# Kernel tuning notes

Hardware: AMD Instinct MI355X
Metric: run time of the kernel (lower is better)

## Reference

```python
import jax, jax.numpy as jnp
import numpy as np

SMOOTH = 1.0      # self.smooth
NUM_ITER = 10     # iter_
EPS = 1e-07
INF = 1e12        # stand-in for +inf in squared-distance init


def _maxpool(x, window):
    # torch max_pool3d(stride=1, padding=w//2): pad with -inf, window max
    pads = ((0, 0), (0, 0)) + tuple((w // 2, w // 2) for w in window)
    return jax.lax.reduce_window(x, -jnp.inf, jax.lax.max, (1, 1) + window, (1, 1, 1, 1, 1), pads)


def _soft_erode(x):  # x: [B,1,D,H,W]
    p1 = -_maxpool(-x, (3, 1, 1))
    p2 = -_maxpool(-x, (1, 3, 1))
    p3 = -_maxpool(-x, (1, 1, 3))
    return jnp.minimum(jnp.minimum(p1, p2), p3)


def _soft_open(x):
    return _maxpool(_soft_erode(x), (3, 3, 3))  # dilate(erode(x))


def _soft_skel(x, n_iter):
    skel = jax.nn.relu(x - _soft_open(x))
    for _ in range(n_iter):
        x = _soft_erode(x)
        delta = jax.nn.relu(x - _soft_open(x))
        skel = skel + jax.nn.relu(delta - skel * delta)
    return skel


def _edt_pass(d2, axis):
    # 1D squared-distance min-convolution: out[i] = min_j (i-j)^2 + d2[j]
    L = d2.shape[axis]
    d2m = jnp.moveaxis(d2, axis, -1)                 # [..., L]
    i = jnp.arange(L, dtype=d2.dtype)
    sq = (i[:, None] - i[None, :]) ** 2              # [L, L]
    out = jnp.min(d2m[..., None, :] + sq, axis=-1)   # [..., L]
    return jnp.moveaxis(out, -1, axis)


def _edt(mask):
    # exact Euclidean distance transform: distance of nonzero voxels to nearest zero voxel
    d2 = jnp.where(mask > 0, INF, 0.0).astype(jnp.float32)  # [B,D,H,W]
    for ax in (1, 2, 3):
        d2 = _edt_pass(d2, ax)
    return jnp.sqrt(d2)


def _get_weights(mask, skel):
    # mask, skel: [B,D,H,W] binary float
    dist = _edt(mask)
    dist = jnp.where(mask == 0, 0.0, dist)
    on_skel = skel == 1
    skel_r = jnp.where(on_skel, dist, 0.0)
    rmax = jnp.max(skel_r.reshape(skel_r.shape[0], -1), axis=1).reshape(-1, 1, 1, 1)
    valid = rmax > 0
    rmax_safe = jnp.where(valid, rmax, 1.0)
    dist_n = jnp.where(valid, dist / rmax_safe, dist)
    skel_rn = jnp.where(valid, skel_r / rmax_safe, skel_r)
    # dim == 3 branch: skel_1_R2_norm
    skel_1r2 = jnp.where(on_skel, (1.0 + EPS) / (skel_rn ** 2 + EPS), 0.0)
    return dist_n, skel_rn, skel_1r2


def _combine(A, B, C):
    # D = B*C, overwritten by A*C where (A != 0) & (B == 0)
    return jnp.where((A != 0) & (B == 0), A * C, B * C)


def reference(y_pred, y_true):
    # y_pred: [B,C,D,H,W] logits; y_true: [B,1,D,H,W] int labels
    fore = jnp.max(y_pred[:, 1:], axis=1, keepdims=True)
    logits = jnp.concatenate([y_pred[:, :1], fore], axis=1)   # [B,2,D,H,W]
    prob = jax.nn.softmax(logits, axis=1)
    yp = (prob[:, 1] > 0.5).astype(jnp.float32)               # [B,D,H,W]
    yt = (y_true > 0).astype(jnp.float32)[:, 0]               # [B,D,H,W]

    skel_p = _soft_skel(yp[:, None], NUM_ITER)[:, 0]
    skel_t = _soft_skel(yt[:, None], NUM_ITER)[:, 0]

    q_vl, q_slvl, q_sl = _get_weights(yt, skel_t)
    q_vp, q_spvp, q_sp = _get_weights(yp, skel_p)

    w_tprec = (jnp.sum(q_sp * q_vl) + SMOOTH) / (jnp.sum(_combine(q_spvp, q_slvl, q_sp)) + SMOOTH)
    w_tsens = (jnp.sum(q_sl * q_vp) + SMOOTH) / (jnp.sum(_combine(q_slvl, q_spvp, q_sl)) + SMOOTH)
    return 1.0 - 2.0 * (w_tprec * w_tsens) / (w_tprec + w_tsens)


def setup_inputs() -> dict:
    key = jax.random.key(0)
    k1, k2 = jax.random.split(key)
    y_pred = jax.random.normal(k1, (2, 2, 64, 96, 96), dtype=jnp.float32)
    y_true = jax.random.randint(k2, (2, 1, 64, 96, 96), 0, 2, dtype=jnp.int32)
    return {"y_pred": y_pred, "y_true": y_true}
```

## Files before the change

### kernel.cpp

```cpp
#include <hip/hip_runtime.h>

namespace {

constexpr int Bn = 2;
constexpr int Dn = 64;
constexpr int Hn = 96;
constexpr int Wn = 96;
constexpr int HW = Hn * Wn;
constexpr int S  = Dn * HW;
constexpr int NBS = Bn * S;
constexpr int NT  = 2 * NBS;
constexpr int WPP = HW / 32;
constexpr int WPS = S / 32;
constexpr int NTW = NT / 32;
constexpr float EPSf = 1e-7f;
constexpr int BLK_SUMS = NBS / 4 / 256;
#define BIGF 1e12f
constexpr int LINF = 1 << 20;

__global__ __launch_bounds__(256) void k_bin0(const float* __restrict__ logits,
                                              const int* __restrict__ labels,
                                              unsigned short* __restrict__ FZ,
                                              unsigned char* __restrict__ DZ) {
  __shared__ unsigned bits[64];
  __shared__ unsigned zlo[32], zhi[32];
  int slab = blockIdx.x / 288;
  int cg = blockIdx.x - slab * 288;
  int c0 = cg * 32;
  int tid = threadIdx.x;
  int lane = tid & 63;
  for (int t = tid; t < 2048; t += 256) {
    int zz = t >> 5;
    int col = t & 31;
    int s = zz * HW + c0 + col;
    bool v;
    if (slab < 2) {
      float l0 = logits[(slab * 2 + 0) * S + s];
      float l1 = logits[(slab * 2 + 1) * S + s];
      v = l1 > l0;
    } else {
      v = labels[(slab - 2) * S + s] > 0;
    }
    unsigned long long m = __ballot(v);
    if (lane == 0)       bits[zz] = (unsigned)m;
    else if (lane == 32) bits[zz] = (unsigned)(m >> 32);
  }
  __syncthreads();
  if (tid < 64) {
    int col = tid & 31;
    int base = (tid < 32) ? 0 : 32;
    unsigned zw = 0u;
    #pragma unroll
    for (int j = 0; j < 32; ++j)
      zw |= (((bits[base + j] >> col) & 1u) ^ 1u) << j;
    if (tid < 32) zlo[col] = zw; else zhi[col] = zw;
  }
  __syncthreads();
  int col = tid & 31;
  int chunk = tid >> 5;
  int i0 = chunk * 8;
  unsigned long long Z = ((unsigned long long)zhi[col] << 32) | (unsigned long long)zlo[col];
  unsigned short* o = FZ + slab * S + c0 + col;
  unsigned char* o1 = DZ + slab * S + c0 + col;
  #pragma unroll
  for (int s = 0; s < 8; ++s) {
    int i = i0 + s;
    unsigned long long below = Z & ((2ull << i) - 1ull);
    unsigned long long above = Z >> i;
    unsigned short fv;
    unsigned char dv;
    if (below | above) {
      int ddn = below ? (i - (63 - __builtin_clzll(below))) : 99;
      int dup = above ? __builtin_ctzll(above) : 99;
      int d = ddn < dup ? ddn : dup;
      fv = (unsigned short)(d * d);
      dv = (unsigned char)d;
    } else {
      fv = 0xFFFFu;
      dv = 255;
    }
    o[i * HW] = fv;
    o1[i * HW] = dv;
  }
}

__global__ __launch_bounds__(256) void k_edtl1(const unsigned short* __restrict__ FZ,
                                               const unsigned char* __restrict__ DZ,
                                               float* __restrict__ EF,
                                               unsigned char* __restrict__ D1) {
  __shared__ __align__(16) unsigned shm[8640];
  unsigned short* fz = (unsigned short*)shm;
  unsigned char*  dz = (unsigned char*)(shm + 4608);
  unsigned char*  t1 = (unsigned char*)(shm + 6912);
  unsigned short* o1 = (unsigned short*)(shm + 7488);
  unsigned short* Afwd = (unsigned short*)shm;
  unsigned short* Bbwd = (unsigned short*)(shm + 4608);
  int slab = blockIdx.x >> 8;
  int z = (blockIdx.x >> 2) & 63;
  int y0 = (blockIdx.x & 3) * 24;
  int tid = threadIdx.x;
  int pb = slab * S + z * HW;
  {
    const uint4* s4 = (const uint4*)(FZ + pb);
    uint4* d4 = (uint4*)fz;
    for (int t = tid; t < 1152; t += 256) d4[t] = s4[t];
    const uint4* s2 = (const uint4*)(DZ + pb);
    uint4* d2 = (uint4*)(shm + 4608);
    for (int t = tid; t < 576; t += 256) d2[t] = s2[t];
  }
  __syncthreads();
  if (tid < 96) {
    int xx = tid;
    int P = LINF;
    int A[24];
    for (int j = 0; j < y0; ++j) {
      int v = dz[j * 96 + xx]; if (v == 255) v = LINF;
      P = min(P, v - j);
    }
    #pragma unroll
    for (int s = 0; s < 24; ++s) {
      int j = y0 + s;
      int v = dz[j * 96 + xx]; if (v == 255) v = LINF;
      P = min(P, v - j);
      A[s] = j + P;
    }
    int Sv = LINF;
    for (int j = 95; j >= y0 + 24; --j) {
      int v = dz[j * 96 + xx]; if (v == 255) v = LINF;
      Sv = min(Sv, v + j);
    }
    #pragma unroll
    for (int s = 23; s >= 0; --s) {
      int j = y0 + s;
      int v = dz[j * 96 + xx]; if (v == 255) v = LINF;
      Sv = min(Sv, v + j);
      int t = min(A[s], Sv - j);
      t1[s * 96 + xx] = (unsigned char)(t > 254 ? 255 : t);
    }
  }
  __syncthreads();
  for (int v = tid; v < 2304; v += 256) {
    int rr = v / 96;
    int xx = v - rr * 96;
    int y = y0 + rr;
    int r = t1[rr * 96 + xx];
    unsigned short res;
    if (r == 255) {
      res = 0xFFFFu;
    } else {
      int lo = y - r; if (lo < 0) lo = 0;
      int hi = y + r; if (hi > 95) hi = 95;
      int best = 1 << 30;
      for (int j = lo; j <= hi; ++j) {
        unsigned short f = fz[j * 96 + xx];
        if (f != 0xFFFFu) {
          int dd = y - j;
          best = min(best, dd * dd + (int)f);
        }
      }
      res = (unsigned short)best;
    }
    o1[rr * 96 + xx] = res;
  }
  __syncthreads();
  if (tid < 24) {
    int rr = tid;
    int P = LINF;
    for (int j = 0; j < 96; ++j) {
      int v = t1[rr * 96 + j]; if (v == 255) v = LINF;
      P = min(P, v - j);
      int a = j + P;
      Afwd[rr * 96 + j] = (unsigned short)(a > 60000 ? 60000 : a);
    }
  }
  if (tid >= 64 && tid < 88) {
    int rr = tid - 64;
    int Sv = LINF;
    for (int j = 95; j >= 0; --j) {
      int v = t1[rr * 96 + j]; if (v == 255) v = LINF;
      Sv = min(Sv, v + j);
      int b = Sv - j;
      Bbwd[rr * 96 + j] = (unsigned short)(b > 60000 ? 60000 : b);
    }
  }
  __syncthreads();
  for (int v = tid; v < 2304; v += 256) {
    int rr = v / 96;
    int x = v - rr * 96;
    int d1v = min((int)Afwd[rr * 96 + x], (int)Bbwd[rr * 96 + x]);
    float outf;
    int d1c;
    if (d1v > 253) {
      outf = BIGF;
      d1c = 12;
    } else {
      d1c = d1v < 12 ? d1v : 12;
      int lo = x - d1v; if (lo < 0) lo = 0;
      int hi = x + d1v; if (hi > 95) hi = 95;
      int best = 1 << 30;
      for (int j = lo; j <= hi; ++j) {
        unsigned short f = o1[rr * 96 + j];
        if (f != 0xFFFFu) {
          int dd = x - j;
          best = min(best, dd * dd + (int)f);
        }
      }
      outf = (float)best;
    }
    int gb = pb + (y0 + rr) * 96 + x;
    EF[gb] = outf;
    D1[gb] = (unsigned char)d1c;
  }
}

__global__ __launch_bounds__(256) void k_skelmax(const unsigned char* __restrict__ D1,
                                                 const float* __restrict__ EF,
                                                 unsigned* __restrict__ SKELB,
                                                 float* __restrict__ pmax) {
  __shared__ unsigned char zm[26 * 96];
  __shared__ unsigned char cen[26 * 96];
  __shared__ float ldsf[4];
  int slab = blockIdx.x >> 8;
  int z = (blockIdx.x >> 2) & 63;
  int y0 = (blockIdx.x & 3) * 24;
  int tid = threadIdx.x;
  int pb = slab * S + z * HW;
  for (int t = tid; t < 2496; t += 256) {
    int rr = t / 96;
    int x = t - rr * 96;
    int yy = y0 - 1 + rr;
    unsigned char m = 0, cv = 0;
    if (yy >= 0 && yy < Hn) {
      int base = slab * S + yy * 96 + x;
      cv = D1[base + z * HW];
      m = cv;
      if (z > 0) { unsigned char a = D1[base + (z - 1) * HW]; m = m > a ? m : a; }
      if (z < Dn - 1) { unsigned char a = D1[base + (z + 1) * HW]; m = m > a ? m : a; }
    }
    zm[t] = m;
    cen[t] = cv;
  }
  __syncthreads();
  float mm = 0.0f;
  int wbase = slab * WPS + z * WPP + y0 * 3;
  int lane = tid & 63;
  #pragma unroll
  for (int round = 0; round < 9; ++round) {
    int v = round * 256 + tid;
    int rr = v / 96;
    int x = v - rr * 96;
    int b1 = rr * 96 + x;
    unsigned char mx = zm[b1];
    { unsigned char a = zm[b1 + 96]; mx = mx > a ? mx : a; }
    { unsigned char a = zm[b1 + 192]; mx = mx > a ? mx : a; }
    if (x > 0) {
      unsigned char a0 = zm[b1 - 1], a1 = zm[b1 + 95], a2 = zm[b1 + 191];
      unsigned char a = a0 > a1 ? a0 : a1; a = a > a2 ? a : a2;
      mx = mx > a ? mx : a;
    }
    if (x < Wn - 1) {
      unsigned char a0 = zm[b1 + 1], a1 = zm[b1 + 97], a2 = zm[b1 + 193];
      unsigned char a = a0 > a1 ? a0 : a1; a = a > a2 ? a : a2;
      mx = mx > a ? mx : a;
    }
    unsigned char d1 = cen[b1 + 96];
    bool sk = (d1 == mx) && (d1 >= 1) && (d1 <= 11);
    unsigned long long bal = __ballot(sk);
    if (lane == 0)       SKELB[wbase + (v >> 5)] = (unsigned)bal;
    else if (lane == 32) SKELB[wbase + (v >> 5)] = (unsigned)(bal >> 32);
    if (sk) mm = fmaxf(mm, EF[pb + (y0 + rr) * 96 + x]);
  }
  #pragma unroll
  for (int o = 32; o > 0; o >>= 1) mm = fmaxf(mm, __shfl_xor(mm, o, 64));
  if (lane == 0) ldsf[tid >> 6] = mm;
  __syncthreads();
  if (tid == 0)
    pmax[blockIdx.x] = fmaxf(fmaxf(ldsf[0], ldsf[1]), fmaxf(ldsf[2], ldsf[3]));
}

__global__ __launch_bounds__(256) void k_sums(const float* __restrict__ d2,
                                              const unsigned* __restrict__ skel,
                                              const float* __restrict__ pmax,
                                              double* __restrict__ ps) {
  __shared__ float lmax[4];
  __shared__ double ldsd[4][4];
  int tid = threadIdx.x;
  {
    int wave = tid >> 6, lane = tid & 63;
    const float* pw = pmax + wave * 256;
    float v = fmaxf(fmaxf(pw[lane], pw[lane + 64]),
                    fmaxf(pw[lane + 128], pw[lane + 192]));
    #pragma unroll
    for (int o = 32; o > 0; o >>= 1) v = fmaxf(v, __shfl_xor(v, o, 64));
    if (lane == 0) lmax[wave] = v;
  }
  __syncthreads();
  int q = blockIdx.x * 256 + tid;
  int idx0 = q * 4;
  int b = idx0 / S;
  float rmax_p = sqrtf(lmax[b]);
  float rmax_t = sqrtf(lmax[2 + b]);
  float4 dp4 = ((const float4*)d2)[q];
  float4 dt4 = ((const float4*)(d2 + NBS))[q];
  unsigned spw = (skel[idx0 >> 5] >> (idx0 & 31)) & 0xFu;
  unsigned stw = (skel[(NBS + idx0) >> 5] >> (idx0 & 31)) & 0xFu;
  const float* dp = &dp4.x;
  const float* dt = &dt4.x;
  double acc[4] = {0.0, 0.0, 0.0, 0.0};
  #pragma unroll
  for (int s = 0; s < 4; ++s) {
    float dist_p = sqrtf(dp[s]);
    float dist_t = sqrtf(dt[s]);
    bool sp = (spw >> s) & 1u;
    bool st = (stw >> s) & 1u;
    float q_vp = (rmax_p > 0.0f) ? dist_p / rmax_p : dist_p;
    float q_vl = (rmax_t > 0.0f) ? dist_t / rmax_t : dist_t;
    float q_spvp = sp ? q_vp : 0.0f;
    float q_slvl = st ? q_vl : 0.0f;
    float q_sp = sp ? (1.0f + EPSf) / (q_spvp * q_spvp + EPSf) : 0.0f;
    float q_sl = st ? (1.0f + EPSf) / (q_slvl * q_slvl + EPSf) : 0.0f;
    acc[0] += (double)(q_sp * q_vl);
    acc[1] += (double)(((q_spvp != 0.0f) && (q_slvl == 0.0f)) ? q_spvp * q_sp
                                                              : q_slvl * q_sp);
    acc[2] += (double)(q_sl * q_vp);
    acc[3] += (double)(((q_slvl != 0.0f) && (q_spvp == 0.0f)) ? q_slvl * q_sl
                                                              : q_spvp * q_sl);
  }
  #pragma unroll
  for (int k = 0; k < 4; ++k)
    #pragma unroll
    for (int o = 32; o > 0; o >>= 1)
      acc[k] += __shfl_xor(acc[k], o, 64);
  if ((tid & 63) == 0) {
    #pragma unroll
    for (int k = 0; k < 4; ++k) ldsd[tid >> 6][k] = acc[k];
  }
  __syncthreads();
  if (tid == 0) {
    #pragma unroll
    for (int k = 0; k < 4; ++k)
      ps[blockIdx.x * 4 + k] = ldsd[0][k] + ldsd[1][k] + ldsd[2][k] + ldsd[3][k];
  }
}

__global__ __launch_bounds__(256) void k_final(const double* __restrict__ ps,
                                               float* __restrict__ out) {
  __shared__ double ldsd[4][4];
  int tid = threadIdx.x;
  double s[4] = {0.0, 0.0, 0.0, 0.0};
  for (int i = tid; i < BLK_SUMS; i += 256) {
    s[0] += ps[i * 4 + 0];
    s[1] += ps[i * 4 + 1];
    s[2] += ps[i * 4 + 2];
    s[3] += ps[i * 4 + 3];
  }
  #pragma unroll
  for (int k = 0; k < 4; ++k)
    #pragma unroll
    for (int o = 32; o > 0; o >>= 1)
      s[k] += __shfl_xor(s[k], o, 64);
  if ((tid & 63) == 0) {
    #pragma unroll
    for (int k = 0; k < 4; ++k) ldsd[tid >> 6][k] = s[k];
  }
  __syncthreads();
  if (tid == 0) {
    double tot[4];
    #pragma unroll
    for (int k = 0; k < 4; ++k)
      tot[k] = ldsd[0][k] + ldsd[1][k] + ldsd[2][k] + ldsd[3][k];
    double wp = (tot[0] + 1.0) / (tot[1] + 1.0);
    double ws = (tot[2] + 1.0) / (tot[3] + 1.0);
    out[0] = (float)(1.0 - 2.0 * (wp * ws) / (wp + ws));
  }
}

}

extern "C" void kernel_launch(void* const* d_in, const int* in_sizes, int n_in,
                              void* d_out, int out_size, void* d_ws, size_t ws_size,
                              hipStream_t stream) {
  (void)in_sizes; (void)n_in; (void)out_size; (void)ws_size;
  const float* logits = (const float*)d_in[0];
  const int* labels   = (const int*)d_in[1];
  float* out = (float*)d_out;

  float* EF = (float*)d_ws;
  unsigned short* FZ = (unsigned short*)(EF + NT);
  unsigned char* DZ  = (unsigned char*)(FZ + NT);
  unsigned char* D1  = DZ + NT;
  unsigned* SKELB = (unsigned*)(D1 + NT);
  float* PMAX  = (float*)(SKELB + NTW);
  double* PS   = (double*)(PMAX + 1024);

  k_bin0<<<1152, 256, 0, stream>>>(logits, labels, FZ, DZ);
  k_edtl1<<<1024, 256, 0, stream>>>(FZ, DZ, EF, D1);
  k_skelmax<<<1024, 256, 0, stream>>>(D1, EF, SKELB, PMAX);
  k_sums<<<1152, 256, 0, stream>>>(EF, SKELB, PMAX, PS);
  k_final<<<1, 256, 0, stream>>>(PS, out);
}
```

Measured before the change: 118.2 us.

## Store squared EDT as u16, fuse final reduction, remap blocks per XCD

Squared distances are now stored as 16-bit integers with 0xFFFF as the infinity sentinel, which halves the traffic for writing and reading the distance field. The per-block max buffer is replaced by atomicMax into a small per-slab array, and the separate final kernel is folded into k_sums through a last-block counter, removing one launch. Block indices are remapped so that neighbouring z slices land on the same XCD to improve L2 locality. The forward and backward row scans in the first EDT pass now run in different thread groups, which costs an extra barrier. Counters are reset inside k_bin0, and the result is only correct if the squared distances fit in 16 bits.

After: 146.1 us. +23.6%, slower.

```diff
diff --git a/kernel.cpp b/kernel.cpp
--- a/kernel.cpp
+++ b/kernel.cpp
@@ -21,9 +21,11 @@
 __global__ __launch_bounds__(256) void k_bin0(const float* __restrict__ logits,
                                               const int* __restrict__ labels,
                                               unsigned short* __restrict__ FZ,
-                                              unsigned char* __restrict__ DZ) {
+                                              unsigned char* __restrict__ DZ,
+                                              unsigned* __restrict__ RMX) {
   __shared__ unsigned bits[64];
   __shared__ unsigned zlo[32], zhi[32];
+  if (blockIdx.x == 0 && threadIdx.x < 8) RMX[threadIdx.x] = 0u;
   int slab = blockIdx.x / 288;
   int cg = blockIdx.x - slab * 288;
   int c0 = cg * 32;
@@ -86,18 +88,23 @@
 
 __global__ __launch_bounds__(256) void k_edtl1(const unsigned short* __restrict__ FZ,
                                                const unsigned char* __restrict__ DZ,
-                                               float* __restrict__ EF,
+                                               unsigned short* __restrict__ E2,
                                                unsigned char* __restrict__ D1) {
   __shared__ __align__(16) unsigned shm[8640];
   unsigned short* fz = (unsigned short*)shm;
   unsigned char*  dz = (unsigned char*)(shm + 4608);
   unsigned char*  t1 = (unsigned char*)(shm + 6912);
   unsigned short* o1 = (unsigned short*)(shm + 7488);
+  unsigned short* Bv = o1;
   unsigned short* Afwd = (unsigned short*)shm;
   unsigned short* Bbwd = (unsigned short*)(shm + 4608);
-  int slab = blockIdx.x >> 8;
-  int z = (blockIdx.x >> 2) & 63;
-  int y0 = (blockIdx.x & 3) * 24;
+  int xcd = blockIdx.x & 7;
+  int inner = blockIdx.x >> 3;
+  int q = inner & 3;
+  int zoff = (inner >> 2) & 7;
+  int slab = inner >> 5;
+  int z = xcd * 8 + zoff;
+  int y0 = q * 24;
   int tid = threadIdx.x;
   int pb = slab * S + z * HW;
   {
@@ -109,10 +116,10 @@
     for (int t = tid; t < 576; t += 256) d2[t] = s2[t];
   }
   __syncthreads();
+  int A[24];
   if (tid < 96) {
     int xx = tid;
     int P = LINF;
-    int A[24];
     for (int j = 0; j < y0; ++j) {
       int v = dz[j * 96 + xx]; if (v == 255) v = LINF;
       P = min(P, v - j);
@@ -124,17 +131,25 @@
       P = min(P, v - j);
       A[s] = j + P;
     }
+  }
+  if (tid >= 128 && tid < 224) {
+    int xx = tid - 128;
     int Sv = LINF;
-    for (int j = 95; j >= y0 + 24; --j) {
+    for (int j = 95; j >= y0; --j) {
       int v = dz[j * 96 + xx]; if (v == 255) v = LINF;
       Sv = min(Sv, v + j);
-    }
-    #pragma unroll
-    for (int s = 23; s >= 0; --s) {
-      int j = y0 + s;
-      int v = dz[j * 96 + xx]; if (v == 255) v = LINF;
-      Sv = min(Sv, v + j);
-      int t = min(A[s], Sv - j);
+      if (j < y0 + 24) {
+        int b = Sv - j;
+        Bv[(j - y0) * 96 + xx] = (unsigned short)(b > 60000 ? 60000 : b);
+      }
+    }
+  }
+  __syncthreads();
+  if (tid < 96) {
+    int xx = tid;
+    #pragma unroll
+    for (int s = 0; s < 24; ++s) {
+      int t = min(A[s], (int)Bv[s * 96 + xx]);
       t1[s * 96 + xx] = (unsigned char)(t > 254 ? 255 : t);
     }
   }
@@ -188,10 +203,10 @@
     int rr = v / 96;
     int x = v - rr * 96;
     int d1v = min((int)Afwd[rr * 96 + x], (int)Bbwd[rr * 96 + x]);
-    float outf;
+    unsigned short oute;
     int d1c;
     if (d1v > 253) {
-      outf = BIGF;
+      oute = 0xFFFFu;
       d1c = 12;
     } else {
       d1c = d1v < 12 ? d1v : 12;
@@ -205,24 +220,28 @@
           best = min(best, dd * dd + (int)f);
         }
       }
-      outf = (float)best;
+      oute = (unsigned short)best;
     }
     int gb = pb + (y0 + rr) * 96 + x;
-    EF[gb] = outf;
+    E2[gb] = oute;
     D1[gb] = (unsigned char)d1c;
   }
 }
 
 __global__ __launch_bounds__(256) void k_skelmax(const unsigned char* __restrict__ D1,
-                                                 const float* __restrict__ EF,
+                                                 const unsigned short* __restrict__ E2,
                                                  unsigned* __restrict__ SKELB,
-                                                 float* __restrict__ pmax) {
+                                                 unsigned* __restrict__ RMX) {
   __shared__ unsigned char zm[26 * 96];
   __shared__ unsigned char cen[26 * 96];
-  __shared__ float ldsf[4];
-  int slab = blockIdx.x >> 8;
-  int z = (blockIdx.x >> 2) & 63;
-  int y0 = (blockIdx.x & 3) * 24;
+  __shared__ unsigned ldsu[4];
+  int xcd = blockIdx.x & 7;
+  int inner = blockIdx.x >> 3;
+  int q = inner & 3;
+  int zoff = (inner >> 2) & 7;
+  int slab = inner >> 5;
+  int z = xcd * 8 + zoff;
+  int y0 = q * 24;
   int tid = threadIdx.x;
   int pb = slab * S + z * HW;
   for (int t = tid; t < 2496; t += 256) {
@@ -241,7 +260,7 @@
     cen[t] = cv;
   }
   __syncthreads();
-  float mm = 0.0f;
+  unsigned mm = 0u;
   int wbase = slab * WPS + z * WPP + y0 * 3;
   int lane = tid & 63;
   #pragma unroll
@@ -268,49 +287,54 @@
     unsigned long long bal = __ballot(sk);
     if (lane == 0)       SKELB[wbase + (v >> 5)] = (unsigned)bal;
     else if (lane == 32) SKELB[wbase + (v >> 5)] = (unsigned)(bal >> 32);
-    if (sk) mm = fmaxf(mm, EF[pb + (y0 + rr) * 96 + x]);
+    if (sk) {
+      unsigned e = E2[pb + (y0 + rr) * 96 + x];
+      mm = mm > e ? mm : e;
+    }
   }
   #pragma unroll
-  for (int o = 32; o > 0; o >>= 1) mm = fmaxf(mm, __shfl_xor(mm, o, 64));
-  if (lane == 0) ldsf[tid >> 6] = mm;
-  __syncthreads();
-  if (tid == 0)
-    pmax[blockIdx.x] = fmaxf(fmaxf(ldsf[0], ldsf[1]), fmaxf(ldsf[2], ldsf[3]));
-}
-
-__global__ __launch_bounds__(256) void k_sums(const float* __restrict__ d2,
+  for (int o = 32; o > 0; o >>= 1) {
+    unsigned t = __shfl_xor(mm, o, 64);
+    mm = mm > t ? mm : t;
+  }
+  if (lane == 0) ldsu[tid >> 6] = mm;
+  __syncthreads();
+  if (tid == 0) {
+    unsigned a = ldsu[0] > ldsu[1] ? ldsu[0] : ldsu[1];
+    unsigned b = ldsu[2] > ldsu[3] ? ldsu[2] : ldsu[3];
+    unsigned m4 = a > b ? a : b;
+    if (m4 > 0u) atomicMax(RMX + slab, m4);
+  }
+}
+
+__global__ __launch_bounds__(256) void k_sums(const unsigned short* __restrict__ E2,
                                               const unsigned* __restrict__ skel,
-                                              const float* __restrict__ pmax,
-                                              double* __restrict__ ps) {
-  __shared__ float lmax[4];
+                                              unsigned* __restrict__ RMX,
+                                              double* __restrict__ ps,
+                                              float* __restrict__ out) {
   __shared__ double ldsd[4][4];
+  __shared__ int lastFlag;
   int tid = threadIdx.x;
-  {
-    int wave = tid >> 6, lane = tid & 63;
-    const float* pw = pmax + wave * 256;
-    float v = fmaxf(fmaxf(pw[lane], pw[lane + 64]),
-                    fmaxf(pw[lane + 128], pw[lane + 192]));
-    #pragma unroll
-    for (int o = 32; o > 0; o >>= 1) v = fmaxf(v, __shfl_xor(v, o, 64));
-    if (lane == 0) lmax[wave] = v;
-  }
-  __syncthreads();
   int q = blockIdx.x * 256 + tid;
   int idx0 = q * 4;
   int b = idx0 / S;
-  float rmax_p = sqrtf(lmax[b]);
-  float rmax_t = sqrtf(lmax[2 + b]);
-  float4 dp4 = ((const float4*)d2)[q];
-  float4 dt4 = ((const float4*)(d2 + NBS))[q];
+  float rmax_p = sqrtf((float)RMX[b]);
+  float rmax_t = sqrtf((float)RMX[2 + b]);
+  ushort4 dp4 = ((const ushort4*)E2)[q];
+  ushort4 dt4 = ((const ushort4*)E2)[q + NBS / 4];
   unsigned spw = (skel[idx0 >> 5] >> (idx0 & 31)) & 0xFu;
   unsigned stw = (skel[(NBS + idx0) >> 5] >> (idx0 & 31)) & 0xFu;
-  const float* dp = &dp4.x;
-  const float* dt = &dt4.x;
+  const unsigned short* dp = &dp4.x;
+  const unsigned short* dt = &dt4.x;
   double acc[4] = {0.0, 0.0, 0.0, 0.0};
   #pragma unroll
   for (int s = 0; s < 4; ++s) {
-    float dist_p = sqrtf(dp[s]);
-    float dist_t = sqrtf(dt[s]);
+    unsigned pv = dp[s];
+    unsigned tv = dt[s];
+    float pd2 = (pv == 0xFFFFu) ? BIGF : (float)pv;
+    float td2 = (tv == 0xFFFFu) ? BIGF : (float)tv;
+    float dist_p = sqrtf(pd2);
+    float dist_t = sqrtf(td2);
     bool sp = (spw >> s) & 1u;
     bool st = (stw >> s) & 1u;
     float q_vp = (rmax_p > 0.0f) ? dist_p / rmax_p : dist_p;
@@ -340,38 +364,39 @@
     #pragma unroll
     for (int k = 0; k < 4; ++k)
       ps[blockIdx.x * 4 + k] = ldsd[0][k] + ldsd[1][k] + ldsd[2][k] + ldsd[3][k];
-  }
-}
-
-__global__ __launch_bounds__(256) void k_final(const double* __restrict__ ps,
-                                               float* __restrict__ out) {
-  __shared__ double ldsd[4][4];
-  int tid = threadIdx.x;
-  double s[4] = {0.0, 0.0, 0.0, 0.0};
-  for (int i = tid; i < BLK_SUMS; i += 256) {
-    s[0] += ps[i * 4 + 0];
-    s[1] += ps[i * 4 + 1];
-    s[2] += ps[i * 4 + 2];
-    s[3] += ps[i * 4 + 3];
-  }
-  #pragma unroll
-  for (int k = 0; k < 4; ++k)
-    #pragma unroll
-    for (int o = 32; o > 0; o >>= 1)
-      s[k] += __shfl_xor(s[k], o, 64);
-  if ((tid & 63) == 0) {
-    #pragma unroll
-    for (int k = 0; k < 4; ++k) ldsd[tid >> 6][k] = s[k];
-  }
-  __syncthreads();
-  if (tid == 0) {
-    double tot[4];
+    __threadfence();
+    unsigned old = atomicAdd(RMX + 4, 1u);
+    lastFlag = (old == (unsigned)(BLK_SUMS - 1));
+  }
+  __syncthreads();
+  if (lastFlag) {
+    __threadfence();
+    double s4[4] = {0.0, 0.0, 0.0, 0.0};
+    for (int i = tid; i < BLK_SUMS; i += 256) {
+      s4[0] += ps[i * 4 + 0];
+      s4[1] += ps[i * 4 + 1];
+      s4[2] += ps[i * 4 + 2];
+      s4[3] += ps[i * 4 + 3];
+    }
     #pragma unroll
     for (int k = 0; k < 4; ++k)
-      tot[k] = ldsd[0][k] + ldsd[1][k] + ldsd[2][k] + ldsd[3][k];
-    double wp = (tot[0] + 1.0) / (tot[1] + 1.0);
-    double ws = (tot[2] + 1.0) / (tot[3] + 1.0);
-    out[0] = (float)(1.0 - 2.0 * (wp * ws) / (wp + ws));
+      #pragma unroll
+      for (int o = 32; o > 0; o >>= 1)
+        s4[k] += __shfl_xor(s4[k], o, 64);
+    if ((tid & 63) == 0) {
+      #pragma unroll
+      for (int k = 0; k < 4; ++k) ldsd[tid >> 6][k] = s4[k];
+    }
+    __syncthreads();
+    if (tid == 0) {
+      double tot[4];
+      #pragma unroll
+      for (int k = 0; k < 4; ++k)
+        tot[k] = ldsd[0][k] + ldsd[1][k] + ldsd[2][k] + ldsd[3][k];
+      double wp = (tot[0] + 1.0) / (tot[1] + 1.0);
+      double wsn = (tot[2] + 1.0) / (tot[3] + 1.0);
+      out[0] = (float)(1.0 - 2.0 * (wp * wsn) / (wp + wsn));
+    }
   }
 }
 
@@ -385,17 +410,16 @@
   const int* labels   = (const int*)d_in[1];
   float* out = (float*)d_out;
 
-  float* EF = (float*)d_ws;
-  unsigned short* FZ = (unsigned short*)(EF + NT);
+  unsigned short* E2 = (unsigned short*)d_ws;
+  unsigned short* FZ = E2 + NT;
   unsigned char* DZ  = (unsigned char*)(FZ + NT);
   unsigned char* D1  = DZ + NT;
   unsigned* SKELB = (unsigned*)(D1 + NT);
-  float* PMAX  = (float*)(SKELB + NTW);
-  double* PS   = (double*)(PMAX + 1024);
-
-  k_bin0<<<1152, 256, 0, stream>>>(logits, labels, FZ, DZ);
-  k_edtl1<<<1024, 256, 0, stream>>>(FZ, DZ, EF, D1);
-  k_skelmax<<<1024, 256, 0, stream>>>(D1, EF, SKELB, PMAX);
-  k_sums<<<1152, 256, 0, stream>>>(EF, SKELB, PMAX, PS);
-  k_final<<<1, 256, 0, stream>>>(PS, out);
-}
+  unsigned* RMX   = SKELB + NTW;
+  double* PS      = (double*)(RMX + 8);
+
+  k_bin0<<<1152, 256, 0, stream>>>(logits, labels, FZ, DZ, RMX);
+  k_edtl1<<<1024, 256, 0, stream>>>(FZ, DZ, E2, D1);
+  k_skelmax<<<1024, 256, 0, stream>>>(D1, E2, SKELB, RMX);
+  k_sums<<<1152, 256, 0, stream>>>(E2, SKELB, RMX, PS, out);
+}
```
